# Kernel optimization log

Hardware: AMD Instinct MI355X
Metric: run time of the kernel (lower is better)

Reference implementation:

```python
import jax, jax.numpy as jnp
import numpy as np


def _seg_softmax(z, seg, num_seg):
    # PyG-style softmax over segments (numerically stable)
    m = jax.ops.segment_max(z, seg, num_segments=num_seg)
    e = jnp.exp(z - m[seg])
    s = jax.ops.segment_sum(e, seg, num_segments=num_seg)
    return e / s[seg]


def _structure(x, W, b, edge_index, batch):
    """Eager (numpy) watershed structure: peaks + level-synchronous BFS fill.
    Faithful to Clusterer.forward/fill: peaks are nodes whose elevation >= all
    in-neighbors; BFS expands along descending edges, a node joins the
    cluster(s) of whichever frontier origins reach it first (ties -> all),
    and is never re-assigned afterwards. Index structure is non-differentiable
    (matches torch autograd semantics)."""
    x = np.asarray(x); W = np.asarray(W); b = np.asarray(b)
    ei = np.asarray(edge_index); batch = np.asarray(batch)
    N = x.shape[0]; B = int(batch.max()) + 1
    # elevation = softmax(Linear(x), batch)
    z = (x @ W.T).ravel() + b[0]
    m = np.full(B, -np.inf, dtype=np.float64); np.maximum.at(m, batch, z)
    e = np.exp(z - m[batch]); s = np.zeros(B); np.add.at(s, batch, e)
    elev = e / s[batch]
    src, dst = ei[0], ei[1]
    # peaks: every incoming edge (src->dst) has elev[dst] >= elev[src]
    deg = np.bincount(dst, minlength=N)
    ge = np.bincount(dst[elev[dst] >= elev[src]], minlength=N)
    peaks = np.nonzero(ge == deg)[0]  # sorted, includes isolated nodes
    # descending edges only
    dmask = elev[dst] <= elev[src]
    ds, dd = src[dmask], dst[dmask]
    mems_list = [peaks]; ids_list = [peaks]
    visited = np.zeros(N, dtype=bool); visited[peaks] = True
    fn, fc = peaks, peaks  # frontier (node, cluster-id) pairs
    while fn.size:
        order = np.argsort(fn, kind='stable')
        fcs = fc[order]
        counts = np.bincount(fn, minlength=N)
        starts = np.concatenate([np.zeros(1, np.int64), np.cumsum(counts)])
        emask = counts[ds] > 0
        es, ed = ds[emask], dd[emask]
        rep = counts[es]
        tot = int(rep.sum())
        if tot == 0:
            break
        # attribute each descent edge to every cluster id of its origin
        base = np.repeat(starts[es], rep)
        grp = np.cumsum(rep) - rep
        within = np.arange(tot) - np.repeat(grp, rep)
        nc = fcs[base + within]
        nd = np.repeat(ed, rep)
        keep = ~visited[nd]  # nodes already in a cluster are never re-assigned
        nd, nc = nd[keep], nc[keep]
        if nd.size == 0:
            break
        pairs = np.unique(np.stack([nd, nc], axis=1), axis=0)
        nd, nc = pairs[:, 0], pairs[:, 1]
        visited[nd] = True
        mems_list.append(nd); ids_list.append(nc)
        fn, fc = nd, nc
    mems = np.concatenate(mems_list)
    ids = np.concatenate(ids_list)
    new_ids = np.searchsorted(peaks, ids)  # relabel peak node ids -> 0..P-1
    cluster_batch = batch[peaks]
    return mems, new_ids, peaks, cluster_batch, int(peaks.size), B


def setup_inputs() -> dict:
    rng = np.random.default_rng(0)
    N, C, B = 100000, 256, 8
    Ng = N // B
    Eu = 800000  # undirected edge draws, ~avg degree 16 after symmetrization
    g = rng.integers(0, B, Eu)
    s = g * Ng + rng.integers(0, Ng, Eu)
    d = g * Ng + rng.integers(0, Ng, Eu)
    keep = s != d
    s, d = s[keep], d[keep]
    src = np.concatenate([s, d]); dst = np.concatenate([d, s])
    key = src * N + dst
    _, idx = np.unique(key, return_index=True)  # coalesce (sorted, deduped)
    edge_index = np.stack([src[idx], dst[idx]]).astype(np.int64)
    batch = np.repeat(np.arange(B), Ng).astype(np.int64)
    x = rng.standard_normal((N, C)).astype(np.float32)
    W = (rng.standard_normal((1, C)) * 0.05).astype(np.float32)
    b = np.zeros((1,), np.float32)
    return {"x": jnp.asarray(x), "edge_index": jnp.asarray(edge_index),
            "batch": jnp.asarray(batch), "W": jnp.asarray(W), "b": jnp.asarray(b)}


def reference(x, edge_index, batch, W, b):
    mems, ids, peaks, cbatch, P, B = _structure(x, W, b, edge_index, batch)
    mems_j = jnp.asarray(mems); ids_j = jnp.asarray(ids); cb = jnp.asarray(cbatch)
    # differentiable pooling math (TopoPool.get_elevations + TopoPool.scale)
    z = (x @ W.T)[:, 0] + b[0]                       # [N]
    elev = _seg_softmax(z, batch, B)                  # per-graph softmax
    max_elev = jax.ops.segment_max(elev[mems_j], ids_j, num_segments=P)   # [P]
    max_x = jax.ops.segment_max(x[mems_j], ids_j, num_segments=P)        # [P,C]
    normed = _seg_softmax(max_elev, cb, B)            # softmax over clusters per graph
    pooled = max_x * normed[:, None]                  # [P,C]
    return pooled, cb, elev
```

## Files before the change

### kernel.cpp

```cpp
#include <hip/hip_runtime.h>
#include <hip/hip_bf16.h>
#include <stdint.h>


#define LINF 0x3FFFFFFF
#define MAXL 60
#define LSPLIT 10
#define NGMAX 12544
#define TAILCAP 8192

__device__ __forceinline__ unsigned encf(float f) {
  unsigned u = __float_as_uint(f);
  return (u & 0x80000000u) ? ~u : (u | 0x80000000u);
}
__device__ __forceinline__ float decf(unsigned u) {
  unsigned v = (u & 0x80000000u) ? (u & 0x7fffffffu) : ~u;
  return __uint_as_float(v);
}
__device__ __forceinline__ float bf2f(unsigned h) {
  return __uint_as_float(h << 16);
}
__device__ __forceinline__ unsigned f2bf(float f) {
  unsigned u = __float_as_uint(f);
  return (u + 0x7FFFu + ((u >> 16) & 1u)) >> 16;
}

__global__ void k_z(const float* __restrict__ x, const float* __restrict__ W,
                    const float* __restrict__ b, const int* __restrict__ batch,
                    float* __restrict__ z, unsigned* __restrict__ bmax_enc,
                    unsigned short* __restrict__ M, int N, int C) {
  __shared__ unsigned smax[8];
  if (threadIdx.x < 8) smax[threadIdx.x] = 0u;
  __syncthreads();
  int lane = threadIdx.x & 63;
  int wid = threadIdx.x >> 6;
  int chunk = (N + gridDim.x - 1) / gridDim.x;
  int v0 = blockIdx.x * chunk;
  int v1 = min(v0 + chunk, N);
  float b0 = b[0];
  for (int v = v0 + (wid << 2); v < v1; v += 16) {
    int nv = min(4, v1 - v);
    float acc[4] = {0.f, 0.f, 0.f, 0.f};
    for (int f = lane * 4; f < C; f += 256) {
      float4 xv[4];
      #pragma unroll
      for (int k = 0; k < 4; ++k) {
        int vv = v + (k < nv ? k : 0);
        xv[k] = *(const float4*)(x + (size_t)vv * C + f);
      }
      float4 wv = *(const float4*)(W + f);
      #pragma unroll
      for (int k = 0; k < 4; ++k) {
        acc[k] += xv[k].x * wv.x + xv[k].y * wv.y + xv[k].z * wv.z + xv[k].w * wv.w;
      }
      #pragma unroll
      for (int k = 0; k < 4; ++k) {
        if (k < nv) {
          uint2 pk;
          pk.x = f2bf(xv[k].x) | (f2bf(xv[k].y) << 16);
          pk.y = f2bf(xv[k].z) | (f2bf(xv[k].w) << 16);
          *(uint2*)(M + (size_t)(v + k) * C + f) = pk;
        }
      }
    }
    #pragma unroll
    for (int off = 32; off > 0; off >>= 1) {
      acc[0] += __shfl_xor(acc[0], off, 64);
      acc[1] += __shfl_xor(acc[1], off, 64);
      acc[2] += __shfl_xor(acc[2], off, 64);
      acc[3] += __shfl_xor(acc[3], off, 64);
    }
    if (lane < nv) {
      float zv = acc[lane] + b0;
      z[v + lane] = zv;
      atomicMax(&smax[batch[v + lane] & 7], encf(zv));
    }
  }
  __syncthreads();
  if (threadIdx.x < 8)
    if (smax[threadIdx.x]) atomicMax(&bmax_enc[threadIdx.x], smax[threadIdx.x]);
}

__global__ void k_e(const float* __restrict__ z, const int* __restrict__ batch,
                    const unsigned* __restrict__ bmax_enc, float* __restrict__ e,
                    float* __restrict__ bsum, int N) {
  __shared__ float ssum[1024];
  for (int i = threadIdx.x; i < 1024; i += blockDim.x) ssum[i] = 0.f;
  __syncthreads();
  int i = blockIdx.x * blockDim.x + threadIdx.x;
  if (i < N) {
    int bt = batch[i] & 1023;
    float ev = expf(z[i] - decf(bmax_enc[bt]));
    e[i] = ev;
    atomicAdd(&ssum[bt], ev);
  }
  __syncthreads();
  for (int t = threadIdx.x; t < 1024; t += blockDim.x)
    if (ssum[t] != 0.f) atomicAdd(&bsum[t], ssum[t]);
}

__global__ void k_edges(const int* __restrict__ ei, const float* __restrict__ z,
                        int* __restrict__ notpeak, int* __restrict__ desc_cnt,
                        const float* __restrict__ e, const float* __restrict__ bsum,
                        const int* __restrict__ batch, float* __restrict__ elev_out,
                        int E, int N) {
  int i = blockIdx.x * blockDim.x + threadIdx.x;
  if (i < N) elev_out[i] = e[i] / bsum[batch[i] & 1023];
  if (i >= E) return;
  int s = ei[i], d = ei[E + i];
  float zs = z[s], zd = z[d];
  if (zd < zs) notpeak[d] = 1;
  if (zd <= zs) atomicAdd(&desc_cnt[s], 1);
}

__global__ void k_chunksum2(const int* __restrict__ desc_cnt, const int* __restrict__ notpeak,
                            int n, int* __restrict__ csA, int* __restrict__ csB) {
  __shared__ int sA[512], sB[512];
  int t = threadIdx.x;
  int i = blockIdx.x * 512 + t;
  int a = 0, bb = 0;
  if (i < n) { a = desc_cnt[i]; bb = (notpeak[i] == 0) ? 1 : 0; }
  sA[t] = a; sB[t] = bb;
  __syncthreads();
  for (int off = 256; off > 0; off >>= 1) {
    if (t < off) { sA[t] += sA[t + off]; sB[t] += sB[t + off]; }
    __syncthreads();
  }
  if (t == 0) { csA[blockIdx.x] = sA[0]; csB[blockIdx.x] = sB[0]; }
}

__global__ void k_chunkscan2(int* __restrict__ csA, int* __restrict__ csB, int nchunks) {
  __shared__ int sA[1024], sB[1024];
  int t = threadIdx.x;
  int vA = (t < nchunks) ? csA[t] : 0;
  int vB = (t < nchunks) ? csB[t] : 0;
  sA[t] = vA; sB[t] = vB;
  __syncthreads();
  for (int off = 1; off < 1024; off <<= 1) {
    int aA = (t >= off) ? sA[t - off] : 0;
    int aB = (t >= off) ? sB[t - off] : 0;
    __syncthreads();
    sA[t] += aA; sB[t] += aB;
    __syncthreads();
  }
  if (t < nchunks) { csA[t] = sA[t] - vA; csB[t] = sB[t] - vB; }
}

__global__ void k_offsets(const int* __restrict__ vals, const int* __restrict__ chunkoff,
                          int2* __restrict__ ocp, int* __restrict__ cursor, int n) {
  __shared__ int s[512];
  int t = threadIdx.x;
  int i = blockIdx.x * 512 + t;
  int v = (i < n) ? vals[i] : 0;
  s[t] = v;
  __syncthreads();
  for (int off = 1; off < 512; off <<= 1) {
    int add = (t >= off) ? s[t - off] : 0;
    __syncthreads();
    s[t] += add;
    __syncthreads();
  }
  if (i < n) {
    int excl = s[t] - v + chunkoff[blockIdx.x];
    ocp[i] = make_int2(excl, excl);
    cursor[i] = excl;
  }
}

__global__ void k_peak_emit(const int* __restrict__ notpeak, const int* __restrict__ chunkoff,
                            const int* __restrict__ batch, const float* __restrict__ elev,
                            int* __restrict__ peaklist, int* __restrict__ cbatch,
                            float* __restrict__ out_cb, float* __restrict__ melev,
                            int n, int P) {
  __shared__ int s[512];
  int t = threadIdx.x;
  int i = blockIdx.x * 512 + t;
  int v = (i < n) ? (notpeak[i] == 0 ? 1 : 0) : 0;
  s[t] = v;
  __syncthreads();
  for (int off = 1; off < 512; off <<= 1) {
    int add = (t >= off) ? s[t - off] : 0;
    __syncthreads();
    s[t] += add;
    __syncthreads();
  }
  if (i < n && v) {
    int r = s[t] - 1 + chunkoff[blockIdx.x];
    if (r < P) {
      peaklist[r] = i;
      int bt = batch[i];
      cbatch[r] = bt;
      out_cb[r] = (float)bt;
      melev[r] = elev[i];
    }
  }
}

__global__ void k_fill(const int* __restrict__ ei, const float* __restrict__ z,
                       int* __restrict__ cursor, unsigned short* __restrict__ adj16,
                       int E, int Ng) {
  int i = blockIdx.x * blockDim.x + threadIdx.x;
  if (i >= E) return;
  int s = ei[i], d = ei[E + i];
  if (z[d] <= z[s]) {
    int pos = atomicAdd(&cursor[s], 1);
    adj16[pos] = (unsigned short)(d % Ng);
  }
}

__global__ void __launch_bounds__(1024, 1)
k_levels(const unsigned short* __restrict__ adj16, const int2* __restrict__ ocp,
         const int* __restrict__ desc_cnt, const int* __restrict__ notpeak,
         int* __restrict__ level, int* __restrict__ lnodes,
         int* __restrict__ qend_g, int Ng, int N) {
  __shared__ int lvl[NGMAX];
  __shared__ unsigned short lq[NGMAX];
  __shared__ int soff[NGMAX + 1];
  __shared__ int s_qcnt[64];
  __shared__ int qend_s[64];
  const int b = blockIdx.x, base = b * Ng;
  const int tid = threadIdx.x, nth = blockDim.x;

  if (tid < 64) s_qcnt[tid] = 0;
  __syncthreads();
  for (int i = tid; i < Ng; i += nth) {
    soff[i] = ocp[base + i].x;
    bool pk = (notpeak[base + i] == 0);
    lvl[i] = pk ? 0 : LINF;
    if (pk) { int p = atomicAdd(&s_qcnt[0], 1); lq[p] = (unsigned short)i; }
  }
  if (tid == 0)
    soff[Ng] = (base + Ng < N) ? ocp[base + Ng].x : (ocp[N - 1].x + desc_cnt[N - 1]);
  {
    int e0 = ocp[base].x;
    int e1 = (base + Ng < N) ? ocp[base + Ng].x : (ocp[N - 1].x + desc_cnt[N - 1]);
    unsigned acc = 0;
    const char* ap = (const char*)adj16;
    for (long byteo = (long)e0 * 2 + (long)tid * 64; byteo < (long)e1 * 2;
         byteo += (long)nth * 64)
      acc += *(const unsigned*)(ap + (byteo & ~(long)3));
    asm volatile("" :: "v"(acc));
  }
  __syncthreads();
  int qb = 0, qe = s_qcnt[0];
  int L = 0;
  while (L < MAXL && qe > qb) {
    if (tid == 0) qend_s[L] = qe;
    int units = (qe - qb) << 2;
    for (int t = tid; t < units; t += nth) {
      int qi = qb + (t >> 2), sub = t & 3;
      int lu = (int)lq[qi];
      int o = soff[lu], oe = soff[lu + 1];
      int j = o + sub;
      if (j < oe) {
        int w0 = adj16[j];
        for (;;) {
          int jn = j + 4;
          int w1 = (jn < oe) ? adj16[jn] : 0;
          int wl = w0;
          if (lvl[wl] == LINF) {
            int old = atomicMin(&lvl[wl], L + 1);
            if (old == LINF) {
              int p = qe + atomicAdd(&s_qcnt[L + 1], 1);
              lq[p] = (unsigned short)wl;
            }
          }
          if (jn >= oe) break;
          w0 = w1; j = jn;
        }
      }
    }
    __syncthreads();
    int produced = s_qcnt[L + 1];
    qb = qe; qe += produced; ++L;
  }
  if (tid == 0) {
    for (int l = L; l < 63; ++l) qend_s[l] = qe;
    qend_s[63] = L;
  }
  __syncthreads();
  if (tid < 64) qend_g[b * 64 + tid] = qend_s[tid];
  for (int i = tid; i < Ng; i += nth) level[base + i] = lvl[i];
  for (int qi = tid; qi < qe; qi += nth) lnodes[base + qi] = (int)lq[qi];
}

__global__ void k_filter(const int* __restrict__ ei, const float* __restrict__ z,
                         const int* __restrict__ level, int2* __restrict__ ocp,
                         unsigned short* __restrict__ adj16, int E, int Ng) {
  int i = blockIdx.x * blockDim.x + threadIdx.x;
  if (i >= E) return;
  int s = ei[i], d = ei[E + i];
  if (z[d] <= z[s] && level[d] == level[s] + 1) {
    int pos = atomicAdd(&ocp[s].y, 1);
    adj16[pos] = (unsigned short)(d % Ng);
  }
}

__global__ void __launch_bounds__(1024, 1)
k_dp_deep(const int* __restrict__ lnodes, const int* __restrict__ qend_g,
          const int2* __restrict__ ocp, const unsigned short* __restrict__ adj16,
          unsigned short* __restrict__ M, int Ng, int C) {
  __shared__ unsigned short lqd[TAILCAP];
  __shared__ int2 soc[TAILCAP];
  __shared__ int qend_s[64];
  const int b = blockIdx.x, base = b * Ng;
  const int tid = threadIdx.x, nth = blockDim.x;
  if (tid < 64) qend_s[tid] = qend_g[b * 64 + tid];
  __syncthreads();
  const int Lmax = qend_s[63];
  if (Lmax - 1 < LSPLIT) return;
  const int ts = qend_s[LSPLIT - 1];
  const int qe = qend_s[62];
  const int tn = qe - ts;
  const bool useCache = (tn > 0) && (tn <= TAILCAP);
  if (useCache) {
    for (int i = tid; i < tn; i += nth) {
      int lid = lnodes[base + ts + i];
      lqd[i] = (unsigned short)lid;
      soc[i] = ocp[base + lid];
    }
  }
  __syncthreads();
  const int lane = tid & 31, hw = tid >> 5, nhw = nth >> 5;
  for (int L2 = Lmax - 1; L2 >= LSPLIT; --L2) {
    int sL = qend_s[L2 - 1], eL = qend_s[L2];
    for (int p = sL + hw; p < eL; p += nhw) {
      int u, o, e2;
      if (useCache) { u = base + (int)lqd[p - ts]; int2 v = soc[p - ts]; o = v.x; e2 = v.y; }
      else          { int lid = lnodes[base + p]; u = base + lid; int2 v = ocp[u]; o = v.x; e2 = v.y; }
      if (e2 == o) continue;
      uint4 sq = ((const uint4*)(M + (size_t)u * C))[lane];
      float4 a0, a1;
      a0.x = bf2f(sq.x & 0xffffu); a0.y = bf2f(sq.x >> 16);
      a0.z = bf2f(sq.y & 0xffffu); a0.w = bf2f(sq.y >> 16);
      a1.x = bf2f(sq.z & 0xffffu); a1.y = bf2f(sq.z >> 16);
      a1.z = bf2f(sq.w & 0xffffu); a1.w = bf2f(sq.w >> 16);
      for (int j = o; j < e2; ++j) {
        int wn = base + (int)adj16[j];
        uint4 q = ((const uint4*)(M + (size_t)wn * C))[lane];
        a0.x = fmaxf(a0.x, bf2f(q.x & 0xffffu));
        a0.y = fmaxf(a0.y, bf2f(q.x >> 16));
        a0.z = fmaxf(a0.z, bf2f(q.y & 0xffffu));
        a0.w = fmaxf(a0.w, bf2f(q.y >> 16));
        a1.x = fmaxf(a1.x, bf2f(q.z & 0xffffu));
        a1.y = fmaxf(a1.y, bf2f(q.z >> 16));
        a1.z = fmaxf(a1.z, bf2f(q.w & 0xffffu));
        a1.w = fmaxf(a1.w, bf2f(q.w >> 16));
      }
      uint4 pk4;
      pk4.x = f2bf(a0.x) | (f2bf(a0.y) << 16);
      pk4.y = f2bf(a0.z) | (f2bf(a0.w) << 16);
      pk4.z = f2bf(a1.x) | (f2bf(a1.y) << 16);
      pk4.w = f2bf(a1.z) | (f2bf(a1.w) << 16);
      ((uint4*)(M + (size_t)u * C))[lane] = pk4;
    }
    __syncthreads();
  }
}

__global__ void __launch_bounds__(256)
k_dp(const int* __restrict__ lnodes, const int* __restrict__ qend,
     const unsigned short* __restrict__ adj16, const int2* __restrict__ ocp,
     unsigned short* __restrict__ M, int L, int C, int Ng) {
  const int b = blockIdx.y;
  const int bNg = b * Ng;
  int lane = threadIdx.x & 31;
  int ghw = (blockIdx.x * blockDim.x + threadIdx.x) >> 5;
  int nhw = (gridDim.x * blockDim.x) >> 5;
  int s = L ? qend[b * 64 + L - 1] : 0;
  int e = qend[b * 64 + L];
  for (int idx = s + ghw; idx < e; idx += nhw) {
    int u = bNg + lnodes[bNg + idx];
    int2 oc2 = ocp[u];
    int o = oc2.x, oc = oc2.y - oc2.x;
    if (oc == 0) continue;
    uint4 sq = ((const uint4*)(M + (size_t)u * C))[lane];
    float4 a0, a1;
    a0.x = bf2f(sq.x & 0xffffu); a0.y = bf2f(sq.x >> 16);
    a0.z = bf2f(sq.y & 0xffffu); a0.w = bf2f(sq.y >> 16);
    a1.x = bf2f(sq.z & 0xffffu); a1.y = bf2f(sq.z >> 16);
    a1.z = bf2f(sq.w & 0xffffu); a1.w = bf2f(sq.w >> 16);
    for (int j = 0; j < oc; j += 4) {
      int m = oc - j;
      int wn[4];
      #pragma unroll
      for (int k = 0; k < 4; k++)
        wn[k] = bNg + (int)adj16[o + j + (k < m ? k : 0)];
      #pragma unroll
      for (int k = 0; k < 4; k++) {
        uint4 q = ((const uint4*)(M + (size_t)wn[k] * C))[lane];
        a0.x = fmaxf(a0.x, bf2f(q.x & 0xffffu));
        a0.y = fmaxf(a0.y, bf2f(q.x >> 16));
        a0.z = fmaxf(a0.z, bf2f(q.y & 0xffffu));
        a0.w = fmaxf(a0.w, bf2f(q.y >> 16));
        a1.x = fmaxf(a1.x, bf2f(q.z & 0xffffu));
        a1.y = fmaxf(a1.y, bf2f(q.z >> 16));
        a1.z = fmaxf(a1.z, bf2f(q.w & 0xffffu));
        a1.w = fmaxf(a1.w, bf2f(q.w >> 16));
      }
    }
    uint4 p;
    p.x = f2bf(a0.x) | (f2bf(a0.y) << 16);
    p.y = f2bf(a0.z) | (f2bf(a0.w) << 16);
    p.z = f2bf(a1.x) | (f2bf(a1.y) << 16);
    p.w = f2bf(a1.z) | (f2bf(a1.w) << 16);
    ((uint4*)(M + (size_t)u * C))[lane] = p;
  }
}

__global__ void k_cnorm(const float* __restrict__ melev, const int* __restrict__ cbatch,
                        float* __restrict__ normed, int P) {
  __shared__ unsigned cm[1024];
  __shared__ float cs[1024];
  int t = threadIdx.x;
  for (int i = t; i < 1024; i += blockDim.x) { cm[i] = 0u; cs[i] = 0.f; }
  __syncthreads();
  for (int i = t; i < P; i += blockDim.x) atomicMax(&cm[cbatch[i] & 1023], encf(melev[i]));
  __syncthreads();
  for (int i = t; i < P; i += blockDim.x) {
    int bt = cbatch[i] & 1023;
    atomicAdd(&cs[bt], expf(melev[i] - decf(cm[bt])));
  }
  __syncthreads();
  for (int i = t; i < P; i += blockDim.x) {
    int bt = cbatch[i] & 1023;
    normed[i] = expf(melev[i] - decf(cm[bt])) / cs[bt];
  }
}

__global__ void __launch_bounds__(256)
k_dp0_pool(const int* __restrict__ peaklist, const float* __restrict__ normed,
           const unsigned short* __restrict__ adj16, const int2* __restrict__ ocp,
           const int* __restrict__ cbatch, const unsigned short* __restrict__ M,
           float* __restrict__ out, int P, int C, int Ng) {
  int lane = threadIdx.x & 31;
  int ghw = (blockIdx.x * blockDim.x + threadIdx.x) >> 5;
  int nhw = (gridDim.x * blockDim.x) >> 5;
  for (int r = ghw; r < P; r += nhw) {
    int u = peaklist[r];
    int base = cbatch[r] * Ng;
    int2 oc2 = ocp[u];
    int o = oc2.x, oc = oc2.y - oc2.x;
    uint4 sq = ((const uint4*)(M + (size_t)u * C))[lane];
    float4 a0, a1;
    a0.x = bf2f(sq.x & 0xffffu); a0.y = bf2f(sq.x >> 16);
    a0.z = bf2f(sq.y & 0xffffu); a0.w = bf2f(sq.y >> 16);
    a1.x = bf2f(sq.z & 0xffffu); a1.y = bf2f(sq.z >> 16);
    a1.z = bf2f(sq.w & 0xffffu); a1.w = bf2f(sq.w >> 16);
    for (int j = 0; j < oc; j += 4) {
      int m = oc - j;
      int wn[4];
      #pragma unroll
      for (int k = 0; k < 4; k++)
        wn[k] = base + (int)adj16[o + j + (k < m ? k : 0)];
      #pragma unroll
      for (int k = 0; k < 4; k++) {
        uint4 q = ((const uint4*)(M + (size_t)wn[k] * C))[lane];
        a0.x = fmaxf(a0.x, bf2f(q.x & 0xffffu));
        a0.y = fmaxf(a0.y, bf2f(q.x >> 16));
        a0.z = fmaxf(a0.z, bf2f(q.y & 0xffffu));
        a0.w = fmaxf(a0.w, bf2f(q.y >> 16));
        a1.x = fmaxf(a1.x, bf2f(q.z & 0xffffu));
        a1.y = fmaxf(a1.y, bf2f(q.z >> 16));
        a1.z = fmaxf(a1.z, bf2f(q.w & 0xffffu));
        a1.w = fmaxf(a1.w, bf2f(q.w >> 16));
      }
    }
    float nr = normed[r];
    float* orow = out + (size_t)r * C + lane * 8;
    float4 o0 = make_float4(a0.x * nr, a0.y * nr, a0.z * nr, a0.w * nr);
    float4 o1 = make_float4(a1.x * nr, a1.y * nr, a1.z * nr, a1.w * nr);
    ((float4*)orow)[0] = o0;
    ((float4*)orow)[1] = o1;
  }
}

extern "C" void kernel_launch(void* const* d_in, const int* in_sizes, int n_in,
                              void* d_out, int out_size, void* d_ws, size_t ws_size,
                              hipStream_t stream) {
  const float* x = (const float*)d_in[0];
  const int* ei = (const int*)d_in[1];
  const int* batch = (const int*)d_in[2];
  const float* W = (const float*)d_in[3];
  const float* b = (const float*)d_in[4];

  const int N = in_sizes[2];
  const int C = in_sizes[0] / N;
  const int E = in_sizes[1] / 2;
  const int P = (out_size - N) / (C + 1);
  const int B = 8;
  const int Ng = N / B;

  float* out = (float*)d_out;
  float* out_pooled = out;
  float* out_cb = out + (size_t)P * C;
  float* out_elev = out_cb + P;

  char* w = (char*)d_ws;
  size_t off = 0;
  auto alloc = [&](size_t bytes) -> void* {
    off = (off + 255) & ~(size_t)255;
    void* p = (void*)(w + off);
    off += bytes;
    return p;
  };
  size_t zero_begin = 0;
  int* notpeak      = (int*)alloc((size_t)N * 4);
  int* desc_cnt     = (int*)alloc((size_t)N * 4);
  unsigned* bmax    = (unsigned*)alloc(1024 * 4);
  float* bsum       = (float*)alloc(1024 * 4);
  size_t zero_end = off;
  float* z          = (float*)alloc((size_t)N * 4);
  float* e          = (float*)alloc((size_t)N * 4);
  int2* ocp         = (int2*)alloc((size_t)N * 8);
  int* cursor       = (int*)alloc((size_t)N * 4);
  int* level        = (int*)alloc((size_t)N * 4);
  int* lnodes       = (int*)alloc((size_t)N * 4);
  int* qend         = (int*)alloc((size_t)B * 64 * 4);
  const int nchunks = (N + 511) / 512;
  int* csA          = (int*)alloc((size_t)nchunks * 4);
  int* csB          = (int*)alloc((size_t)nchunks * 4);
  int* cbatch       = (int*)alloc((size_t)P * 4);
  float* normed     = (float*)alloc((size_t)P * 4);
  float* melev      = (float*)alloc((size_t)P * 4);
  int* peaklist     = (int*)alloc((size_t)P * 4);
  unsigned short* adj16 = (unsigned short*)alloc((size_t)E * 2);
  unsigned short* M = (unsigned short*)alloc((size_t)N * C * 2);

  hipMemsetAsync(w + zero_begin, 0, zero_end - zero_begin, stream);

  k_z<<<2048, 256, 0, stream>>>(x, W, b, batch, z, bmax, M, N, C);
  int nblkN = (N + 255) / 256;
  k_e<<<nblkN, 256, 0, stream>>>(z, batch, bmax, e, bsum, N);
  int nblkE = (E + 255) / 256;
  k_edges<<<nblkE, 256, 0, stream>>>(ei, z, notpeak, desc_cnt, e, bsum, batch,
                                     out_elev, E, N);
  k_chunksum2<<<nchunks, 512, 0, stream>>>(desc_cnt, notpeak, N, csA, csB);
  k_chunkscan2<<<1, 1024, 0, stream>>>(csA, csB, nchunks);
  k_offsets<<<nchunks, 512, 0, stream>>>(desc_cnt, csA, ocp, cursor, N);
  k_fill<<<nblkE, 256, 0, stream>>>(ei, z, cursor, adj16, E, Ng);
  k_peak_emit<<<nchunks, 512, 0, stream>>>(notpeak, csB, batch, out_elev,
                                           peaklist, cbatch, out_cb, melev, N, P);
  k_cnorm<<<1, 1024, 0, stream>>>(melev, cbatch, normed, P);
  k_levels<<<B, 1024, 0, stream>>>(adj16, ocp, desc_cnt, notpeak, level, lnodes,
                                   qend, Ng, N);
  k_filter<<<nblkE, 256, 0, stream>>>(ei, z, level, ocp, adj16, E, Ng);
  k_dp_deep<<<B, 1024, 0, stream>>>(lnodes, qend, ocp, adj16, M, Ng, C);
  dim3 gdp(256, B);
  for (int L = LSPLIT - 1; L >= 1; --L) {
    k_dp<<<gdp, 256, 0, stream>>>(lnodes, qend, adj16, ocp, M, L, C, Ng);
  }
  k_dp0_pool<<<512, 256, 0, stream>>>(peaklist, normed, adj16, ocp, cbatch, M,
                                      out_pooled, P, C, Ng);
}
```

Before: 498.2 us.

## Build descent CSR by edge-order scan instead of per-source atomics

Replaces the per-node desc_cnt atomics, offset scan and atomic-cursor fill with a block-level stream compaction over the edge list. This relies on edges being sorted by source so that each node's range can be written from run boundaries into ocp.x/y. The filter stage is rebuilt the same way as a sum, scan and scatter, and k_levels now takes per-node counts from ocp instead of a sentinel offset. The aim is to remove global atomic contention and keep the adjacency order deterministic. The cost is extra launches and a hard assumption that edges are grouped by source and that nE fits in 1024 blocks.

New measurement: 412.8 us. 1.21x faster.

```diff
diff --git a/kernel.cpp b/kernel.cpp
--- a/kernel.cpp
+++ b/kernel.cpp
@@ -99,71 +99,114 @@
     if (ssum[t] != 0.f) atomicAdd(&bsum[t], ssum[t]);
 }
 
-__global__ void k_edges(const int* __restrict__ ei, const float* __restrict__ z,
-                        int* __restrict__ notpeak, int* __restrict__ desc_cnt,
-                        const float* __restrict__ e, const float* __restrict__ bsum,
-                        const int* __restrict__ batch, float* __restrict__ elev_out,
-                        int E, int N) {
-  int i = blockIdx.x * blockDim.x + threadIdx.x;
-  if (i < N) elev_out[i] = e[i] / bsum[batch[i] & 1023];
-  if (i >= E) return;
-  int s = ei[i], d = ei[E + i];
-  float zs = z[s], zd = z[d];
-  if (zd < zs) notpeak[d] = 1;
-  if (zd <= zs) atomicAdd(&desc_cnt[s], 1);
-}
-
-__global__ void k_chunksum2(const int* __restrict__ desc_cnt, const int* __restrict__ notpeak,
-                            int n, int* __restrict__ csA, int* __restrict__ csB) {
-  __shared__ int sA[512], sB[512];
+__global__ void __launch_bounds__(1024)
+k_edges(const int* __restrict__ ei, const float* __restrict__ z,
+        int* __restrict__ notpeak, const float* __restrict__ e,
+        const float* __restrict__ bsum, const int* __restrict__ batch,
+        float* __restrict__ elev_out, int* __restrict__ csE,
+        int E, int N, int nE) {
+  __shared__ int sred[1024];
+  int t = threadIdx.x;
+  int i0 = blockIdx.x * 2048 + t;
+  int i1 = i0 + 1024;
+  if (i0 < N) elev_out[i0] = e[i0] / bsum[batch[i0] & 1023];
+  if (i1 < N) elev_out[i1] = e[i1] / bsum[batch[i1] & 1023];
+  int cnt = 0;
+  if (i0 < E) {
+    int s = ei[i0], d = ei[E + i0];
+    float zs = z[s], zd = z[d];
+    if (zd < zs) notpeak[d] = 1;
+    if (zd <= zs) cnt++;
+  }
+  if (i1 < E) {
+    int s = ei[i1], d = ei[E + i1];
+    float zs = z[s], zd = z[d];
+    if (zd < zs) notpeak[d] = 1;
+    if (zd <= zs) cnt++;
+  }
+  sred[t] = cnt;
+  __syncthreads();
+  for (int off = 512; off > 0; off >>= 1) {
+    if (t < off) sred[t] += sred[t + off];
+    __syncthreads();
+  }
+  if (t == 0 && (int)blockIdx.x < nE) csE[blockIdx.x] = sred[0];
+}
+
+__global__ void k_chunksumP(const int* __restrict__ notpeak, int n,
+                            int* __restrict__ csB) {
+  __shared__ int s[512];
   int t = threadIdx.x;
   int i = blockIdx.x * 512 + t;
-  int a = 0, bb = 0;
-  if (i < n) { a = desc_cnt[i]; bb = (notpeak[i] == 0) ? 1 : 0; }
-  sA[t] = a; sB[t] = bb;
+  s[t] = (i < n && notpeak[i] == 0) ? 1 : 0;
   __syncthreads();
   for (int off = 256; off > 0; off >>= 1) {
-    if (t < off) { sA[t] += sA[t + off]; sB[t] += sB[t + off]; }
-    __syncthreads();
-  }
-  if (t == 0) { csA[blockIdx.x] = sA[0]; csB[blockIdx.x] = sB[0]; }
-}
-
-__global__ void k_chunkscan2(int* __restrict__ csA, int* __restrict__ csB, int nchunks) {
-  __shared__ int sA[1024], sB[1024];
-  int t = threadIdx.x;
-  int vA = (t < nchunks) ? csA[t] : 0;
-  int vB = (t < nchunks) ? csB[t] : 0;
-  sA[t] = vA; sB[t] = vB;
-  __syncthreads();
-  for (int off = 1; off < 1024; off <<= 1) {
-    int aA = (t >= off) ? sA[t - off] : 0;
-    int aB = (t >= off) ? sB[t - off] : 0;
-    __syncthreads();
-    sA[t] += aA; sB[t] += aB;
-    __syncthreads();
-  }
-  if (t < nchunks) { csA[t] = sA[t] - vA; csB[t] = sB[t] - vB; }
-}
-
-__global__ void k_offsets(const int* __restrict__ vals, const int* __restrict__ chunkoff,
-                          int2* __restrict__ ocp, int* __restrict__ cursor, int n) {
-  __shared__ int s[512];
-  int t = threadIdx.x;
-  int i = blockIdx.x * 512 + t;
-  int v = (i < n) ? vals[i] : 0;
+    if (t < off) s[t] += s[t + off];
+    __syncthreads();
+  }
+  if (t == 0) csB[blockIdx.x] = s[0];
+}
+
+__global__ void k_scan2(int* __restrict__ csB, int nB, int* __restrict__ csE, int nE) {
+  __shared__ int s[1024];
+  int t = threadIdx.x;
+  int v = (t < nB) ? csB[t] : 0;
   s[t] = v;
   __syncthreads();
-  for (int off = 1; off < 512; off <<= 1) {
-    int add = (t >= off) ? s[t - off] : 0;
-    __syncthreads();
-    s[t] += add;
-    __syncthreads();
-  }
-  if (i < n) {
-    int excl = s[t] - v + chunkoff[blockIdx.x];
-    ocp[i] = make_int2(excl, excl);
-    cursor[i] = excl;
+  for (int o = 1; o < 1024; o <<= 1) {
+    int a = (t >= o) ? s[t - o] : 0;
+    __syncthreads();
+    s[t] += a;
+    __syncthreads();
+  }
+  if (t < nB) csB[t] = s[t] - v;
+  __syncthreads();
+  int v2 = (t < nE) ? csE[t] : 0;
+  s[t] = v2;
+  __syncthreads();
+  for (int o = 1; o < 1024; o <<= 1) {
+    int a = (t >= o) ? s[t - o] : 0;
+    __syncthreads();
+    s[t] += a;
+    __syncthreads();
+  }
+  if (t < nE) csE[t] = s[t] - v2;
+}
+
+__global__ void __launch_bounds__(1024)
+k_efill(const int* __restrict__ ei, const float* __restrict__ z,
+        const int* __restrict__ csE, unsigned short* __restrict__ adj16,
+        int2* __restrict__ ocp, int E, int Ng) {
+  __shared__ int sc[1024];
+  int t = threadIdx.x;
+  int i0 = blockIdx.x * 2048 + 2 * t;
+  int i1 = i0 + 1;
+  int s0 = -1, d0 = 0, s1 = -1, d1 = 0, f0 = 0, f1 = 0;
+  if (i0 < E) { s0 = ei[i0]; d0 = ei[E + i0]; f0 = (z[d0] <= z[s0]) ? 1 : 0; }
+  if (i1 < E) { s1 = ei[i1]; d1 = ei[E + i1]; f1 = (z[d1] <= z[s1]) ? 1 : 0; }
+  sc[t] = f0 + f1;
+  __syncthreads();
+  for (int o = 1; o < 1024; o <<= 1) {
+    int a = (t >= o) ? sc[t - o] : 0;
+    __syncthreads();
+    sc[t] += a;
+    __syncthreads();
+  }
+  int excl = sc[t] - (f0 + f1) + csE[blockIdx.x];
+  if (i0 < E) {
+    int g0 = excl;
+    if (f0) adj16[g0] = (unsigned short)(d0 % Ng);
+    int prev_s = (i0 > 0) ? ei[i0 - 1] : -1;
+    if (s0 != prev_s) ocp[s0].x = g0;
+    int next_s = (i1 < E) ? s1 : -1;
+    if (s0 != next_s) ocp[s0].y = g0 + f0;
+  }
+  if (i1 < E) {
+    int g1 = excl + f0;
+    if (f1) adj16[g1] = (unsigned short)(d1 % Ng);
+    if (s1 != s0) ocp[s1].x = g1;
+    int next_s = (i1 + 1 < E) ? ei[i1 + 1] : -1;
+    if (s1 != next_s) ocp[s1].y = g1 + f1;
   }
 }
 
@@ -196,52 +239,48 @@
   }
 }
 
-__global__ void k_fill(const int* __restrict__ ei, const float* __restrict__ z,
-                       int* __restrict__ cursor, unsigned short* __restrict__ adj16,
-                       int E, int Ng) {
-  int i = blockIdx.x * blockDim.x + threadIdx.x;
-  if (i >= E) return;
-  int s = ei[i], d = ei[E + i];
-  if (z[d] <= z[s]) {
-    int pos = atomicAdd(&cursor[s], 1);
-    adj16[pos] = (unsigned short)(d % Ng);
-  }
-}
-
 __global__ void __launch_bounds__(1024, 1)
 k_levels(const unsigned short* __restrict__ adj16, const int2* __restrict__ ocp,
-         const int* __restrict__ desc_cnt, const int* __restrict__ notpeak,
-         int* __restrict__ level, int* __restrict__ lnodes,
-         int* __restrict__ qend_g, int Ng, int N) {
+         const int* __restrict__ notpeak, int* __restrict__ level,
+         int* __restrict__ lnodes, int* __restrict__ qend_g, int Ng, int N) {
   __shared__ int lvl[NGMAX];
   __shared__ unsigned short lq[NGMAX];
-  __shared__ int soff[NGMAX + 1];
+  __shared__ int soff[NGMAX];
+  __shared__ unsigned short scnt[NGMAX];
   __shared__ int s_qcnt[64];
   __shared__ int qend_s[64];
+  __shared__ int s_lo, s_hi;
   const int b = blockIdx.x, base = b * Ng;
   const int tid = threadIdx.x, nth = blockDim.x;
 
   if (tid < 64) s_qcnt[tid] = 0;
-  __syncthreads();
+  if (tid == 0) { s_lo = 0x7fffffff; s_hi = 0; }
+  __syncthreads();
+  int mylo = 0x7fffffff, myhi = 0;
   for (int i = tid; i < Ng; i += nth) {
-    soff[i] = ocp[base + i].x;
+    int2 v = ocp[base + i];
+    soff[i] = v.x;
+    scnt[i] = (unsigned short)(v.y - v.x);
+    if (v.y > v.x) { mylo = min(mylo, v.x); myhi = max(myhi, v.y); }
     bool pk = (notpeak[base + i] == 0);
     lvl[i] = pk ? 0 : LINF;
     if (pk) { int p = atomicAdd(&s_qcnt[0], 1); lq[p] = (unsigned short)i; }
   }
-  if (tid == 0)
-    soff[Ng] = (base + Ng < N) ? ocp[base + Ng].x : (ocp[N - 1].x + desc_cnt[N - 1]);
+  #pragma unroll
+  for (int o = 32; o > 0; o >>= 1) {
+    mylo = min(mylo, __shfl_xor(mylo, o, 64));
+    myhi = max(myhi, __shfl_xor(myhi, o, 64));
+  }
+  if ((tid & 63) == 0) { atomicMin(&s_lo, mylo); atomicMax(&s_hi, myhi); }
+  __syncthreads();
   {
-    int e0 = ocp[base].x;
-    int e1 = (base + Ng < N) ? ocp[base + Ng].x : (ocp[N - 1].x + desc_cnt[N - 1]);
+    long b0 = (long)s_lo * 2, b1 = (long)s_hi * 2;
     unsigned acc = 0;
     const char* ap = (const char*)adj16;
-    for (long byteo = (long)e0 * 2 + (long)tid * 64; byteo < (long)e1 * 2;
-         byteo += (long)nth * 64)
+    for (long byteo = b0 + (long)tid * 64; byteo < b1; byteo += (long)nth * 64)
       acc += *(const unsigned*)(ap + (byteo & ~(long)3));
     asm volatile("" :: "v"(acc));
   }
-  __syncthreads();
   int qb = 0, qe = s_qcnt[0];
   int L = 0;
   while (L < MAXL && qe > qb) {
@@ -250,7 +289,7 @@
     for (int t = tid; t < units; t += nth) {
       int qi = qb + (t >> 2), sub = t & 3;
       int lu = (int)lq[qi];
-      int o = soff[lu], oe = soff[lu + 1];
+      int o = soff[lu], oe = o + (int)scnt[lu];
       int j = o + sub;
       if (j < oe) {
         int w0 = adj16[j];
@@ -284,15 +323,87 @@
   for (int qi = tid; qi < qe; qi += nth) lnodes[base + qi] = (int)lq[qi];
 }
 
-__global__ void k_filter(const int* __restrict__ ei, const float* __restrict__ z,
-                         const int* __restrict__ level, int2* __restrict__ ocp,
-                         unsigned short* __restrict__ adj16, int E, int Ng) {
-  int i = blockIdx.x * blockDim.x + threadIdx.x;
-  if (i >= E) return;
-  int s = ei[i], d = ei[E + i];
-  if (z[d] <= z[s] && level[d] == level[s] + 1) {
-    int pos = atomicAdd(&ocp[s].y, 1);
-    adj16[pos] = (unsigned short)(d % Ng);
+__global__ void __launch_bounds__(1024)
+k_fsum(const int* __restrict__ ei, const float* __restrict__ z,
+       const int* __restrict__ level, int* __restrict__ csF, int E) {
+  __shared__ int sred[1024];
+  int t = threadIdx.x;
+  int i0 = blockIdx.x * 2048 + t;
+  int i1 = i0 + 1024;
+  int c = 0;
+  if (i0 < E) {
+    int s = ei[i0], d = ei[E + i0];
+    if (z[d] <= z[s] && level[d] == level[s] + 1) c++;
+  }
+  if (i1 < E) {
+    int s = ei[i1], d = ei[E + i1];
+    if (z[d] <= z[s] && level[d] == level[s] + 1) c++;
+  }
+  sred[t] = c;
+  __syncthreads();
+  for (int off = 512; off > 0; off >>= 1) {
+    if (t < off) sred[t] += sred[t + off];
+    __syncthreads();
+  }
+  if (t == 0) csF[blockIdx.x] = sred[0];
+}
+
+__global__ void k_fscan(int* __restrict__ csF, int nE) {
+  __shared__ int s[1024];
+  int t = threadIdx.x;
+  int v = (t < nE) ? csF[t] : 0;
+  s[t] = v;
+  __syncthreads();
+  for (int o = 1; o < 1024; o <<= 1) {
+    int a = (t >= o) ? s[t - o] : 0;
+    __syncthreads();
+    s[t] += a;
+    __syncthreads();
+  }
+  if (t < nE) csF[t] = s[t] - v;
+}
+
+__global__ void __launch_bounds__(1024)
+k_fscatter(const int* __restrict__ ei, const float* __restrict__ z,
+           const int* __restrict__ level, const int* __restrict__ csF,
+           unsigned short* __restrict__ adj16, int2* __restrict__ ocp,
+           int E, int Ng) {
+  __shared__ int sc[1024];
+  int t = threadIdx.x;
+  int i0 = blockIdx.x * 2048 + 2 * t;
+  int i1 = i0 + 1;
+  int s0 = -1, d0 = 0, s1 = -1, d1 = 0, f0 = 0, f1 = 0;
+  if (i0 < E) {
+    s0 = ei[i0]; d0 = ei[E + i0];
+    f0 = (z[d0] <= z[s0] && level[d0] == level[s0] + 1) ? 1 : 0;
+  }
+  if (i1 < E) {
+    s1 = ei[i1]; d1 = ei[E + i1];
+    f1 = (z[d1] <= z[s1] && level[d1] == level[s1] + 1) ? 1 : 0;
+  }
+  sc[t] = f0 + f1;
+  __syncthreads();
+  for (int o = 1; o < 1024; o <<= 1) {
+    int a = (t >= o) ? sc[t - o] : 0;
+    __syncthreads();
+    sc[t] += a;
+    __syncthreads();
+  }
+  int excl = sc[t] - (f0 + f1) + csF[blockIdx.x];
+  if (i0 < E) {
+    int g0 = excl;
+    if (f0) adj16[g0] = (unsigned short)(d0 % Ng);
+    int prev_s = (i0 > 0) ? ei[i0 - 1] : -1;
+    if (s0 != prev_s) ocp[s0].x = g0;
+    int next_s = (i1 < E) ? s1 : -1;
+    if (s0 != next_s) ocp[s0].y = g0 + f0;
+  }
+  if (i1 < E) {
+    int g1 = excl + f0;
+    if (f1) adj16[g1] = (unsigned short)(d1 % Ng);
+    if (s1 != s0) ocp[s1].x = g1;
+    int next_s = (i1 + 1 < E) ? ei[i1 + 1] : -1;
+    if (s1 != next_s) ocp[s1].y = g1 + f1;
   }
 }
 
@@ -506,20 +617,21 @@
   };
   size_t zero_begin = 0;
   int* notpeak      = (int*)alloc((size_t)N * 4);
-  int* desc_cnt     = (int*)alloc((size_t)N * 4);
+  int2* ocp         = (int2*)alloc((size_t)N * 8);
   unsigned* bmax    = (unsigned*)alloc(1024 * 4);
   float* bsum       = (float*)alloc(1024 * 4);
   size_t zero_end = off;
   float* z          = (float*)alloc((size_t)N * 4);
   float* e          = (float*)alloc((size_t)N * 4);
-  int2* ocp         = (int2*)alloc((size_t)N * 8);
-  int* cursor       = (int*)alloc((size_t)N * 4);
   int* level        = (int*)alloc((size_t)N * 4);
   int* lnodes       = (int*)alloc((size_t)N * 4);
   int* qend         = (int*)alloc((size_t)B * 64 * 4);
-  const int nchunks = (N + 511) / 512;
-  int* csA          = (int*)alloc((size_t)nchunks * 4);
-  int* csB          = (int*)alloc((size_t)nchunks * 4);
+  const int nchunksN = (N + 511) / 512;
+  const int nE = (E + 2047) / 2048;
+  const int gE = ((E > N ? E : N) + 2047) / 2048;
+  int* csB          = (int*)alloc((size_t)nchunksN * 4);
+  int* csE          = (int*)alloc((size_t)gE * 4);
+  int* csF          = (int*)alloc((size_t)gE * 4);
   int* cbatch       = (int*)alloc((size_t)P * 4);
   float* normed     = (float*)alloc((size_t)P * 4);
   float* melev      = (float*)alloc((size_t)P * 4);
@@ -532,19 +644,18 @@
   k_z<<<2048, 256, 0, stream>>>(x, W, b, batch, z, bmax, M, N, C);
   int nblkN = (N + 255) / 256;
   k_e<<<nblkN, 256, 0, stream>>>(z, batch, bmax, e, bsum, N);
-  int nblkE = (E + 255) / 256;
-  k_edges<<<nblkE, 256, 0, stream>>>(ei, z, notpeak, desc_cnt, e, bsum, batch,
-                                     out_elev, E, N);
-  k_chunksum2<<<nchunks, 512, 0, stream>>>(desc_cnt, notpeak, N, csA, csB);
-  k_chunkscan2<<<1, 1024, 0, stream>>>(csA, csB, nchunks);
-  k_offsets<<<nchunks, 512, 0, stream>>>(desc_cnt, csA, ocp, cursor, N);
-  k_fill<<<nblkE, 256, 0, stream>>>(ei, z, cursor, adj16, E, Ng);
-  k_peak_emit<<<nchunks, 512, 0, stream>>>(notpeak, csB, batch, out_elev,
-                                           peaklist, cbatch, out_cb, melev, N, P);
+  k_edges<<<gE, 1024, 0, stream>>>(ei, z, notpeak, e, bsum, batch, out_elev,
+                                   csE, E, N, nE);
+  k_chunksumP<<<nchunksN, 512, 0, stream>>>(notpeak, N, csB);
+  k_scan2<<<1, 1024, 0, stream>>>(csB, nchunksN, csE, nE);
+  k_efill<<<nE, 1024, 0, stream>>>(ei, z, csE, adj16, ocp, E, Ng);
+  k_peak_emit<<<nchunksN, 512, 0, stream>>>(notpeak, csB, batch, out_elev,
+                                            peaklist, cbatch, out_cb, melev, N, P);
   k_cnorm<<<1, 1024, 0, stream>>>(melev, cbatch, normed, P);
-  k_levels<<<B, 1024, 0, stream>>>(adj16, ocp, desc_cnt, notpeak, level, lnodes,
-                                   qend, Ng, N);
-  k_filter<<<nblkE, 256, 0, stream>>>(ei, z, level, ocp, adj16, E, Ng);
+  k_levels<<<B, 1024, 0, stream>>>(adj16, ocp, notpeak, level, lnodes, qend, Ng, N);
+  k_fsum<<<nE, 1024, 0, stream>>>(ei, z, level, csF, E);
+  k_fscan<<<1, 1024, 0, stream>>>(csF, nE);
+  k_fscatter<<<nE, 1024, 0, stream>>>(ei, z, level, csF, adj16, ocp, E, Ng);
   k_dp_deep<<<B, 1024, 0, stream>>>(lnodes, qend, ocp, adj16, M, Ng, C);
   dim3 gdp(256, B);
   for (int L = LSPLIT - 1; L >= 1; --L) {
```
